# Kernel optimization log

Hardware: AMD Instinct MI355X
Metric: run time of the kernel (lower is better)

## Reference

```python
import jax, jax.numpy as jnp
import numpy as np

SLOPE = 25.0

@jax.custom_vjp
def spike_fn(u):
    return (u > 0).astype(u.dtype)

def _spike_fwd(u):
    return (u > 0).astype(u.dtype), u

def _spike_bwd(u, g):
    # fast-sigmoid surrogate gradient, slope=25 (matches surrogate_slope)
    return (g / (1.0 + SLOPE * jnp.abs(u)) ** 2,)

spike_fn.defvjp(_spike_fwd, _spike_bwd)

B, T, D = 4, 8192, 1024
TREE_DEPTH = 10
NUM_NODES = (1 << TREE_DEPTH) - 1


def setup_inputs() -> dict:
    key = jax.random.key(0)
    k0, k1, k2 = jax.random.split(key, 3)
    x = jax.random.normal(k0, (B, T, D), jnp.float32)
    # torch Linear(2D -> D, bias=False): weight [D, 2D], kaiming-uniform-ish scale
    W_proj = jax.random.normal(k1, (D, 2 * D), jnp.float32) / np.sqrt(2 * D)
    node_weights = jax.random.normal(k2, (NUM_NODES, D), jnp.float32) * 0.02
    bt = jnp.ones((TREE_DEPTH, D), jnp.float32) * 0.5    # base_threshold per level
    as_w = jnp.ones((TREE_DEPTH, D), jnp.float32) * 0.1  # adapt_strength per level
    rms_w = jnp.ones((D,), jnp.float32)                   # RMSNorm weight
    return {"x": x, "W_proj": W_proj, "node_weights": node_weights,
            "bt": bt, "as_w": as_w, "rms_w": rms_w}


def reference(x, W_proj, node_weights, bt, as_w, rms_w):
    b, t, d = x.shape
    tree_depth = bt.shape[0]
    num_nodes = (1 << tree_depth) - 1

    padded_T = 1 << int(np.ceil(np.log2(t)))
    x_p = jnp.pad(x, ((0, 0), (0, padded_T - t), (0, 0))) if padded_T > t else x

    eff_depth = min(tree_depth, int(np.log2(padded_T)))
    num_leaves = 1 << eff_depth
    sub_seq = padded_T // num_leaves
    # [B, num_leaves, D]: mean-pool sub-sequences into leaf states
    leaves = x_p.reshape(b, num_leaves, sub_seq, d).mean(axis=2)

    node_states = jnp.zeros((b, num_nodes, d), x.dtype)
    leaf_start = (1 << (eff_depth - 1)) - 1
    valid = min(num_leaves, num_nodes - leaf_start)
    node_states = node_states.at[:, leaf_start:leaf_start + valid].set(leaves[:, :valid])

    # bottom-up over tree levels (static small loop over eff_depth)
    for level in range(eff_depth - 1, -1, -1):
        level_start = (1 << level) - 1
        level_end = min((1 << (level + 1)) - 1, num_nodes)
        nodes = np.arange(level_start, level_end)
        mask = 2 * nodes + 1 < num_nodes
        if not mask.any():
            continue  # leaf level: children out of range, write is a no-op
        nsel = nodes[mask]
        l_idx = 2 * nsel + 1
        r_idx = 2 * nsel + 2  # always < num_nodes in a full binary tree when l is
        l_states = node_states[:, l_idx]               # [B, n_lvl, D] gather
        r_states = node_states[:, r_idx]
        fused = jnp.concatenate([l_states, r_states], axis=-1)  # [B, n_lvl, 2D]
        proj = jnp.einsum('bne,de->bnd', fused, W_proj)
        # ALIF single step from zero state: v = proj, thresh = bt (adapt = 0)
        u = proj - (bt[level] + as_w[level] * 0.0)
        spike = spike_fn(u)
        node_states = node_states.at[:, nsel].set(proj * spike)

    weights = jax.nn.softmax(node_weights, axis=0)       # softmax over nodes
    mixture = jnp.einsum('nd,bnd->bd', weights, node_states)
    out = mixture[:, None, :] + x_p[:, :t]               # broadcast over T
    # RMSNorm (torch default eps = machine eps for dtype)
    eps = jnp.finfo(x.dtype).eps
    rms = jnp.sqrt(jnp.mean(out * out, axis=-1, keepdims=True) + eps)
    return (out / rms) * rms_w
```

## Files before the change

### kernel.cpp

```cpp
#include <hip/hip_runtime.h>


#define NODES 1023
#define DIM   1024
#define K2    2048
#define NCHUNK 64

typedef short short8 __attribute__((ext_vector_type(8)));
typedef float floatx4 __attribute__((ext_vector_type(4)));

__device__ __forceinline__ unsigned short f2bf(float f) {
    unsigned u = __float_as_uint(f);
    unsigned r = ((u >> 16) & 1u) + 0x7fffu;
    return (unsigned short)((u + r) >> 16);
}

#define GLD16(g, l)                                                            \
    __builtin_amdgcn_global_load_lds(                                          \
        (const __attribute__((address_space(1))) void*)(g),                    \
        (__attribute__((address_space(3))) void*)(l), 16, 0, 0)

__global__ __launch_bounds__(256) void k_cvt_w(const float* __restrict__ W,
                                               unsigned short* __restrict__ Wb) {
    int i = (blockIdx.x * 256 + threadIdx.x) * 4;
    float4 v = *(const float4*)(W + i);
    ushort4 o;
    o.x = f2bf(v.x); o.y = f2bf(v.y); o.z = f2bf(v.z); o.w = f2bf(v.w);
    *(ushort4*)(Wb + i) = o;
}

__global__ __launch_bounds__(256) void k_leaves(const float* __restrict__ x,
                                                float* __restrict__ Sf,
                                                unsigned short* __restrict__ Sb) {
    int leaf = blockIdx.x;
    int b = blockIdx.y;
    int d = threadIdx.x * 4;
    const float* xp = x + ((size_t)b * 8192 + (size_t)leaf * 8) * DIM + d;
    float4 s = {0.f, 0.f, 0.f, 0.f};
#pragma unroll
    for (int i = 0; i < 8; ++i) {
        float4 v = *(const float4*)(xp + (size_t)i * DIM);
        s.x += v.x; s.y += v.y; s.z += v.z; s.w += v.w;
    }
    s.x *= 0.125f; s.y *= 0.125f; s.z *= 0.125f; s.w *= 0.125f;
    size_t o = ((size_t)b * NODES + 511 + leaf) * DIM + d;
    *(float4*)(Sf + o) = s;
    ushort4 ob; ob.x = f2bf(s.x); ob.y = f2bf(s.y); ob.z = f2bf(s.z); ob.w = f2bf(s.w);
    *(ushort4*)(Sb + o) = ob;
}

__global__ __launch_bounds__(256) void k_level_mfma(
    const unsigned short* __restrict__ SbIn, const unsigned short* __restrict__ Wb,
    const float* __restrict__ bt, float* __restrict__ Sf,
    unsigned short* __restrict__ SbOut, float* __restrict__ P,
    int L, int R, int nit) {
    const int lvl_start = (1 << L) - 1;
    const int child_start = (2 << L) - 1;
    const int mask = (1 << L) - 1;

    __shared__ unsigned short Al[2][128 * 64];
    __shared__ unsigned short Bl[2][128 * 64];

    const int t = threadIdx.x;
    const int lane = t & 63;
    const int w = t >> 6;
    const int wm = w >> 1, wn = w & 1;
    const int bm = blockIdx.y, bn = blockIdx.x;
    const int ksid = blockIdx.z;
    const int k_base = ksid * nit * 64;

    floatx4 acc[4][4];
#pragma unroll
    for (int i = 0; i < 4; ++i)
#pragma unroll
        for (int j = 0; j < 4; ++j) acc[i][j] = (floatx4){0.f, 0.f, 0.f, 0.f};

    const int trow = t >> 3;
    const int tcol = (t & 7) * 8;

    const unsigned short* aptr[4];
#pragma unroll
    for (int p = 0; p < 4; ++p) {
        int rg = bm * 128 + p * 32 + trow;
        rg = rg < R ? rg : R - 1;
        int bb = rg >> L;
        int nl = rg & mask;
        aptr[p] = SbIn + ((size_t)bb * NODES + child_start + 2 * nl) * DIM + tcol;
    }
    const unsigned short* bptr[4];
#pragma unroll
    for (int p = 0; p < 4; ++p) {
        int rg = bn * 128 + p * 32 + trow;
        bptr[p] = Wb + (size_t)rg * K2 + tcol;
    }

#define STAGE(buf, k0)                                                         \
    {                                                                          \
        _Pragma("unroll")                                                      \
        for (int p = 0; p < 4; ++p)                                            \
            GLD16(aptr[p] + (k0), &Al[buf][(p * 32 + w * 8) * 64]);            \
        _Pragma("unroll")                                                      \
        for (int p = 0; p < 4; ++p)                                            \
            GLD16(bptr[p] + (k0), &Bl[buf][(p * 32 + w * 8) * 64]);            \
    }

    int cur = 0;
    STAGE(0, k_base);
    asm volatile("s_waitcnt vmcnt(0)" ::: "memory");
    __builtin_amdgcn_s_barrier();

    for (int it = 0; it < nit; ++it) {
        if (it + 1 < nit) STAGE(cur ^ 1, k_base + (it + 1) * 64);
#pragma unroll
        for (int ks = 0; ks < 2; ++ks) {
            short8 af[4], bf[4];
#pragma unroll
            for (int i = 0; i < 4; ++i) {
                af[i] = *(const short8*)&Al[cur][(wm * 64 + i * 16 + (lane & 15)) * 64 +
                                                ks * 32 + (lane >> 4) * 8];
                bf[i] = *(const short8*)&Bl[cur][(wn * 64 + i * 16 + (lane & 15)) * 64 +
                                                ks * 32 + (lane >> 4) * 8];
            }
#pragma unroll
            for (int i = 0; i < 4; ++i)
#pragma unroll
                for (int j = 0; j < 4; ++j)
                    acc[i][j] = __builtin_amdgcn_mfma_f32_16x16x32_bf16(
                        af[i], bf[j], acc[i][j], 0, 0, 0);
        }
        asm volatile("s_waitcnt vmcnt(0)" ::: "memory");
        __builtin_amdgcn_s_barrier();
        cur ^= 1;
    }
#undef STAGE

    if (P) {
        float* Pr = P + (size_t)ksid * R * DIM;
#pragma unroll
        for (int i = 0; i < 4; ++i)
#pragma unroll
            for (int j = 0; j < 4; ++j)
#pragma unroll
                for (int r = 0; r < 4; ++r) {
                    int m = bm * 128 + wm * 64 + i * 16 + (lane >> 4) * 4 + r;
                    int n = bn * 128 + wn * 64 + j * 16 + (lane & 15);
                    if (m < R) Pr[(size_t)m * DIM + n] = acc[i][j][r];
                }
    } else {
#pragma unroll
        for (int i = 0; i < 4; ++i)
#pragma unroll
            for (int j = 0; j < 4; ++j)
#pragma unroll
                for (int r = 0; r < 4; ++r) {
                    int m = bm * 128 + wm * 64 + i * 16 + (lane >> 4) * 4 + r;
                    int n = bn * 128 + wn * 64 + j * 16 + (lane & 15);
                    if (m < R) {
                        float v = acc[i][j][r];
                        float u = v - bt[L * DIM + n];
                        float o = (u > 0.f) ? v : 0.f;
                        int bb = m >> L;
                        int nl = m & mask;
                        size_t idx = ((size_t)bb * NODES + lvl_start + nl) * DIM + n;
                        Sf[idx] = o;
                        SbOut[idx] = f2bf(o);
                    }
                }
    }
}

__global__ __launch_bounds__(256) void k_level_fix(
    const float* __restrict__ P, const float* __restrict__ bt,
    float* __restrict__ Sf, unsigned short* __restrict__ Sb,
    int L, int R, int KS) {
    int m = blockIdx.x;
    int n = threadIdx.x * 4;
    float4 s = {0.f, 0.f, 0.f, 0.f};
    for (int k = 0; k < KS; ++k) {
        float4 v = *(const float4*)(P + ((size_t)k * R + m) * DIM + n);
        s.x += v.x; s.y += v.y; s.z += v.z; s.w += v.w;
    }
    float4 btv = *(const float4*)(bt + (size_t)L * DIM + n);
    float4 o;
    o.x = (s.x - btv.x > 0.f) ? s.x : 0.f;
    o.y = (s.y - btv.y > 0.f) ? s.y : 0.f;
    o.z = (s.z - btv.z > 0.f) ? s.z : 0.f;
    o.w = (s.w - btv.w > 0.f) ? s.w : 0.f;
    int b = m >> L;
    int nl = m & ((1 << L) - 1);
    size_t idx = ((size_t)b * NODES + ((1 << L) - 1) + nl) * DIM + n;
    *(float4*)(Sf + idx) = o;
    ushort4 ob;
    ob.x = f2bf(o.x); ob.y = f2bf(o.y); ob.z = f2bf(o.z); ob.w = f2bf(o.w);
    *(ushort4*)(Sb + idx) = ob;
}

__global__ __launch_bounds__(256) void k_level_small(
    const float* __restrict__ SfIn, const float* __restrict__ W,
    const float* __restrict__ bt, float* __restrict__ Sf,
    unsigned short* __restrict__ Sb, int L) {
    int r = blockIdx.y;
    int b = r >> L;
    int nl = r & ((1 << L) - 1);
    int node = (1 << L) - 1 + nl;
    int child = 2 * node + 1;
    const float* A = SfIn + ((size_t)b * NODES + child) * DIM;

    __shared__ float Alds[K2];
    int t = threadIdx.x;
    ((float4*)Alds)[t * 2] = ((const float4*)A)[t * 2];
    ((float4*)Alds)[t * 2 + 1] = ((const float4*)A)[t * 2 + 1];
    __syncthreads();

    int d = blockIdx.x * 64 + (t & 63);
    int kc = t >> 6;
    const float4* Wr = (const float4*)(W + (size_t)d * K2 + kc * 512);
    const float4* Ar = (const float4*)(Alds + kc * 512);
    float s = 0.f;
#pragma unroll 8
    for (int i = 0; i < 128; ++i) {
        float4 wv = Wr[i], av = Ar[i];
        s += wv.x * av.x + wv.y * av.y + wv.z * av.z + wv.w * av.w;
    }
    __shared__ float part[256];
    part[t] = s;
    __syncthreads();
    if (t < 64) {
        float v = part[t] + part[t + 64] + part[t + 128] + part[t + 192];
        float u = v - bt[L * DIM + d];
        float o = (u > 0.f) ? v : 0.f;
        size_t idx = ((size_t)b * NODES + node) * DIM + d;
        Sf[idx] = o;
        Sb[idx] = f2bf(o);
    }
}

__global__ __launch_bounds__(256) void k_mixture_part(const float* __restrict__ nw,
                                                      const float* __restrict__ Sf,
                                                      float* __restrict__ part) {
    int d = blockIdx.x * 256 + threadIdx.x;
    int c = blockIdx.y;
    int n0i = c * 16;
    int n1i = n0i + 16 < NODES ? n0i + 16 : NODES;
    float denom = 0.f, s0 = 0.f, s1 = 0.f, s2 = 0.f, s3 = 0.f;
    for (int n = n0i; n < n1i; ++n) {
        float wv = __expf(nw[(size_t)n * DIM + d]);
        denom += wv;
        s0 += wv * Sf[((size_t)0 * NODES + n) * DIM + d];
        s1 += wv * Sf[((size_t)1 * NODES + n) * DIM + d];
        s2 += wv * Sf[((size_t)2 * NODES + n) * DIM + d];
        s3 += wv * Sf[((size_t)3 * NODES + n) * DIM + d];
    }
    size_t base = ((size_t)c * 5) * DIM + d;
    part[base]           = denom;
    part[base + 1 * DIM] = s0;
    part[base + 2 * DIM] = s1;
    part[base + 3 * DIM] = s2;
    part[base + 4 * DIM] = s3;
}

__global__ __launch_bounds__(256) void k_mixture_red(const float* __restrict__ part,
                                                     float* __restrict__ mix) {
    int d = blockIdx.x * 256 + threadIdx.x;
    float denom = 0.f, s0 = 0.f, s1 = 0.f, s2 = 0.f, s3 = 0.f;
#pragma unroll 8
    for (int c = 0; c < NCHUNK; ++c) {
        size_t base = ((size_t)c * 5) * DIM + d;
        denom += part[base];
        s0 += part[base + 1 * DIM];
        s1 += part[base + 2 * DIM];
        s2 += part[base + 3 * DIM];
        s3 += part[base + 4 * DIM];
    }
    float inv = 1.f / denom;
    mix[0 * DIM + d] = s0 * inv;
    mix[1 * DIM + d] = s1 * inv;
    mix[2 * DIM + d] = s2 * inv;
    mix[3 * DIM + d] = s3 * inv;
}

__global__ __launch_bounds__(256) void k_final(const float* __restrict__ x,
                                               const float* __restrict__ mix,
                                               const float* __restrict__ rw,
                                               float* __restrict__ out) {
    int row = blockIdx.x;
    int b = row >> 13;
    size_t base = (size_t)row * DIM;
    int t = threadIdx.x;
    float4 xv = *(const float4*)(x + base + t * 4);
    float4 mv = *(const float4*)(mix + b * DIM + t * 4);
    float4 v = {xv.x + mv.x, xv.y + mv.y, xv.z + mv.z, xv.w + mv.w};
    float ss = v.x * v.x + v.y * v.y + v.z * v.z + v.w * v.w;
#pragma unroll
    for (int o = 32; o > 0; o >>= 1) ss += __shfl_xor(ss, o, 64);
    __shared__ float wsum[4];
    int lane = t & 63, wv_ = t >> 6;
    if (lane == 0) wsum[wv_] = ss;
    __syncthreads();
    float tot = wsum[0] + wsum[1] + wsum[2] + wsum[3];
    float inv = 1.f / sqrtf(tot * (1.f / 1024.f) + 1.1920929e-7f);
    float4 rwv = *(const float4*)(rw + t * 4);
    float4 o4 = {v.x * inv * rwv.x, v.y * inv * rwv.y, v.z * inv * rwv.z,
                 v.w * inv * rwv.w};
    *(float4*)(out + base + t * 4) = o4;
}

extern "C" void kernel_launch(void* const* d_in, const int* in_sizes, int n_in,
                              void* d_out, int out_size, void* d_ws, size_t ws_size,
                              hipStream_t stream) {
    (void)in_sizes; (void)n_in; (void)out_size;
    const float* x  = (const float*)d_in[0];
    const float* W  = (const float*)d_in[1];
    const float* nw = (const float*)d_in[2];
    const float* bt = (const float*)d_in[3];
    const float* rw = (const float*)d_in[5];
    float* out = (float*)d_out;

    char* ws = (char*)d_ws;
    const size_t SF_BYTES = (size_t)4 * NODES * DIM * 4;
    const size_t SB_BYTES = (size_t)4 * NODES * DIM * 2;
    const size_t WB_BYTES = (size_t)K2 * DIM * 2;
    const size_t MIX_BYTES = (size_t)4 * DIM * 4;
    const size_t BASE = SF_BYTES + SB_BYTES + WB_BYTES + MIX_BYTES;
    float* Sf = (float*)ws;
    unsigned short* Sb = (unsigned short*)(ws + SF_BYTES);
    unsigned short* Wb = (unsigned short*)(ws + SF_BYTES + SB_BYTES);
    float* mix = (float*)(ws + SF_BYTES + SB_BYTES + WB_BYTES);
    float* P = (float*)(ws + BASE);
    float* part = (float*)(ws + BASE);
    size_t avail = ws_size > BASE ? ws_size - BASE : 0;

    k_cvt_w<<<2048, 256, 0, stream>>>(W, Wb);
    k_leaves<<<dim3(512, 4), 256, 0, stream>>>(x, Sf, Sb);

    for (int L = 8; L >= 4; --L) {
        int R = 4 << L;
        int Mt = (R + 127) / 128;
        int ks = (L == 8) ? 4 : (L == 7) ? 8 : 16;
        while (ks > 1 && (size_t)ks * R * DIM * 4 > avail) ks >>= 1;
        if (ks >= 2 && (size_t)ks * R * DIM * 4 <= avail) {
            int nit = 32 / ks;
            k_level_mfma<<<dim3(8, Mt, ks), 256, 0, stream>>>(
                Sb, Wb, bt, Sf, Sb, P, L, R, nit);
            k_level_fix<<<R, 256, 0, stream>>>(P, bt, Sf, Sb, L, R, ks);
        } else {
            k_level_mfma<<<dim3(8, Mt, 1), 256, 0, stream>>>(
                Sb, Wb, bt, Sf, Sb, nullptr, L, R, 32);
        }
    }
    for (int L = 3; L >= 0; --L) {
        int R = 4 << L;
        k_level_small<<<dim3(16, R), 256, 0, stream>>>(Sf, W, bt, Sf, Sb, L);
    }
    k_mixture_part<<<dim3(4, NCHUNK), 256, 0, stream>>>(nw, Sf, part);
    k_mixture_red<<<4, 256, 0, stream>>>(part, mix);
    k_final<<<32768, 256, 0, stream>>>(x, mix, rw, out);
}
```

Measured before the change: 444.0 us.

## Shrink MFMA tiles to 64x64, add triple-buffered swizzled LDS, fuse prep kernels

Tiles in the per-level bf16 MFMA GEMM shrink from 128x128 to 64x64 with a three-stage LDS ring and partial vmcnt waits, so the next loads overlap compute. An XOR swizzle on LDS columns is meant to cut bank conflicts on fragment reads. Split-K factors are lowered because the smaller tiles already give more blocks. The weight conversion and leaf pooling kernels are merged into one launch. The trade-off is less data reuse per tile, and small levels may still leave the GPU underfilled.

```diff
diff --git a/kernel.cpp b/kernel.cpp
--- a/kernel.cpp
+++ b/kernel.cpp
@@ -20,33 +20,37 @@
         (const __attribute__((address_space(1))) void*)(g),                    \
         (__attribute__((address_space(3))) void*)(l), 16, 0, 0)
 
-__global__ __launch_bounds__(256) void k_cvt_w(const float* __restrict__ W,
-                                               unsigned short* __restrict__ Wb) {
-    int i = (blockIdx.x * 256 + threadIdx.x) * 4;
-    float4 v = *(const float4*)(W + i);
-    ushort4 o;
-    o.x = f2bf(v.x); o.y = f2bf(v.y); o.z = f2bf(v.z); o.w = f2bf(v.w);
-    *(ushort4*)(Wb + i) = o;
-}
-
-__global__ __launch_bounds__(256) void k_leaves(const float* __restrict__ x,
-                                                float* __restrict__ Sf,
-                                                unsigned short* __restrict__ Sb) {
-    int leaf = blockIdx.x;
-    int b = blockIdx.y;
-    int d = threadIdx.x * 4;
-    const float* xp = x + ((size_t)b * 8192 + (size_t)leaf * 8) * DIM + d;
-    float4 s = {0.f, 0.f, 0.f, 0.f};
-#pragma unroll
-    for (int i = 0; i < 8; ++i) {
-        float4 v = *(const float4*)(xp + (size_t)i * DIM);
-        s.x += v.x; s.y += v.y; s.z += v.z; s.w += v.w;
-    }
-    s.x *= 0.125f; s.y *= 0.125f; s.z *= 0.125f; s.w *= 0.125f;
-    size_t o = ((size_t)b * NODES + 511 + leaf) * DIM + d;
-    *(float4*)(Sf + o) = s;
-    ushort4 ob; ob.x = f2bf(s.x); ob.y = f2bf(s.y); ob.z = f2bf(s.z); ob.w = f2bf(s.w);
-    *(ushort4*)(Sb + o) = ob;
+__global__ __launch_bounds__(256) void k_prep(const float* __restrict__ W,
+                                              unsigned short* __restrict__ Wb,
+                                              const float* __restrict__ x,
+                                              float* __restrict__ Sf,
+                                              unsigned short* __restrict__ Sb) {
+    int bx = blockIdx.x;
+    if (bx < 2048) {
+        int i = (bx * 256 + threadIdx.x) * 4;
+        float4 v = *(const float4*)(W + i);
+        ushort4 o;
+        o.x = f2bf(v.x); o.y = f2bf(v.y); o.z = f2bf(v.z); o.w = f2bf(v.w);
+        *(ushort4*)(Wb + i) = o;
+    } else {
+        int idx = bx - 2048;
+        int leaf = idx & 511;
+        int b = idx >> 9;
+        int d = threadIdx.x * 4;
+        const float* xp = x + ((size_t)b * 8192 + (size_t)leaf * 8) * DIM + d;
+        float4 s = {0.f, 0.f, 0.f, 0.f};
+#pragma unroll
+        for (int i = 0; i < 8; ++i) {
+            float4 v = *(const float4*)(xp + (size_t)i * DIM);
+            s.x += v.x; s.y += v.y; s.z += v.z; s.w += v.w;
+        }
+        s.x *= 0.125f; s.y *= 0.125f; s.z *= 0.125f; s.w *= 0.125f;
+        size_t o = ((size_t)b * NODES + 511 + leaf) * DIM + d;
+        *(float4*)(Sf + o) = s;
+        ushort4 ob;
+        ob.x = f2bf(s.x); ob.y = f2bf(s.y); ob.z = f2bf(s.z); ob.w = f2bf(s.w);
+        *(ushort4*)(Sb + o) = ob;
+    }
 }
 
 __global__ __launch_bounds__(256) void k_level_mfma(
@@ -58,8 +62,8 @@
     const int child_start = (2 << L) - 1;
     const int mask = (1 << L) - 1;
 
-    __shared__ unsigned short Al[2][128 * 64];
-    __shared__ unsigned short Bl[2][128 * 64];
+    __shared__ unsigned short Al[3][64 * 64];
+    __shared__ unsigned short Bl[3][64 * 64];
 
     const int t = threadIdx.x;
     const int lane = t & 63;
@@ -69,92 +73,103 @@
     const int ksid = blockIdx.z;
     const int k_base = ksid * nit * 64;
 
-    floatx4 acc[4][4];
-#pragma unroll
-    for (int i = 0; i < 4; ++i)
-#pragma unroll
-        for (int j = 0; j < 4; ++j) acc[i][j] = (floatx4){0.f, 0.f, 0.f, 0.f};
+    floatx4 acc[2][2];
+#pragma unroll
+    for (int i = 0; i < 2; ++i)
+#pragma unroll
+        for (int j = 0; j < 2; ++j) acc[i][j] = (floatx4){0.f, 0.f, 0.f, 0.f};
 
     const int trow = t >> 3;
-    const int tcol = (t & 7) * 8;
-
-    const unsigned short* aptr[4];
-#pragma unroll
-    for (int p = 0; p < 4; ++p) {
-        int rg = bm * 128 + p * 32 + trow;
+    const int csw = ((t & 7) ^ (trow & 7)) * 8;
+
+    const unsigned short* aptr[2];
+#pragma unroll
+    for (int p = 0; p < 2; ++p) {
+        int rg = bm * 64 + p * 32 + trow;
         rg = rg < R ? rg : R - 1;
         int bb = rg >> L;
         int nl = rg & mask;
-        aptr[p] = SbIn + ((size_t)bb * NODES + child_start + 2 * nl) * DIM + tcol;
-    }
-    const unsigned short* bptr[4];
-#pragma unroll
-    for (int p = 0; p < 4; ++p) {
-        int rg = bn * 128 + p * 32 + trow;
-        bptr[p] = Wb + (size_t)rg * K2 + tcol;
+        aptr[p] = SbIn + ((size_t)bb * NODES + child_start + 2 * nl) * DIM + csw;
+    }
+    const unsigned short* bptr[2];
+#pragma unroll
+    for (int p = 0; p < 2; ++p) {
+        int rg = bn * 64 + p * 32 + trow;
+        bptr[p] = Wb + (size_t)rg * K2 + csw;
     }
 
 #define STAGE(buf, k0)                                                         \
     {                                                                          \
         _Pragma("unroll")                                                      \
-        for (int p = 0; p < 4; ++p)                                            \
+        for (int p = 0; p < 2; ++p)                                            \
             GLD16(aptr[p] + (k0), &Al[buf][(p * 32 + w * 8) * 64]);            \
         _Pragma("unroll")                                                      \
-        for (int p = 0; p < 4; ++p)                                            \
+        for (int p = 0; p < 2; ++p)                                            \
             GLD16(bptr[p] + (k0), &Bl[buf][(p * 32 + w * 8) * 64]);            \
     }
 
-    int cur = 0;
+    const int rsel = lane & 15;
+    const int jx = lane >> 4;
+    const int swz = lane & 7;
+
     STAGE(0, k_base);
-    asm volatile("s_waitcnt vmcnt(0)" ::: "memory");
-    __builtin_amdgcn_s_barrier();
+    if (nit > 1) STAGE(1, k_base + 64);
 
     for (int it = 0; it < nit; ++it) {
-        if (it + 1 < nit) STAGE(cur ^ 1, k_base + (it + 1) * 64);
+        if (it + 1 < nit) {
+            asm volatile("s_waitcnt vmcnt(4)" ::: "memory");
+        } else {
+            asm volatile("s_waitcnt vmcnt(0)" ::: "memory");
+        }
+        __builtin_amdgcn_s_barrier();
+        asm volatile("" ::: "memory");
+        if (it + 2 < nit) STAGE((it + 2) % 3, k_base + (it + 2) * 64);
+
+        const char* Ab = (const char*)&Al[it % 3][0];
+        const char* Bb = (const char*)&Bl[it % 3][0];
 #pragma unroll
         for (int ks = 0; ks < 2; ++ks) {
-            short8 af[4], bf[4];
-#pragma unroll
-            for (int i = 0; i < 4; ++i) {
-                af[i] = *(const short8*)&Al[cur][(wm * 64 + i * 16 + (lane & 15)) * 64 +
-                                                ks * 32 + (lane >> 4) * 8];
-                bf[i] = *(const short8*)&Bl[cur][(wn * 64 + i * 16 + (lane & 15)) * 64 +
-                                                ks * 32 + (lane >> 4) * 8];
+            short8 af[2], bf[2];
+#pragma unroll
+            for (int i = 0; i < 2; ++i) {
+                int ar = wm * 32 + i * 16 + rsel;
+                af[i] = *(const short8*)(Ab + ar * 128 +
+                                         (((ks * 4 + jx) ^ swz) << 4));
+                int br = wn * 32 + i * 16 + rsel;
+                bf[i] = *(const short8*)(Bb + br * 128 +
+                                         (((ks * 4 + jx) ^ swz) << 4));
             }
 #pragma unroll
-            for (int i = 0; i < 4; ++i)
-#pragma unroll
-                for (int j = 0; j < 4; ++j)
+            for (int i = 0; i < 2; ++i)
+#pragma unroll
+                for (int j = 0; j < 2; ++j)
                     acc[i][j] = __builtin_amdgcn_mfma_f32_16x16x32_bf16(
                         af[i], bf[j], acc[i][j], 0, 0, 0);
         }
-        asm volatile("s_waitcnt vmcnt(0)" ::: "memory");
-        __builtin_amdgcn_s_barrier();
-        cur ^= 1;
     }
 #undef STAGE
 
     if (P) {
         float* Pr = P + (size_t)ksid * R * DIM;
 #pragma unroll
-        for (int i = 0; i < 4; ++i)
-#pragma unroll
-            for (int j = 0; j < 4; ++j)
+        for (int i = 0; i < 2; ++i)
+#pragma unroll
+            for (int j = 0; j < 2; ++j)
 #pragma unroll
                 for (int r = 0; r < 4; ++r) {
-                    int m = bm * 128 + wm * 64 + i * 16 + (lane >> 4) * 4 + r;
-                    int n = bn * 128 + wn * 64 + j * 16 + (lane & 15);
+                    int m = bm * 64 + wm * 32 + i * 16 + (lane >> 4) * 4 + r;
+                    int n = bn * 64 + wn * 32 + j * 16 + (lane & 15);
                     if (m < R) Pr[(size_t)m * DIM + n] = acc[i][j][r];
                 }
     } else {
 #pragma unroll
-        for (int i = 0; i < 4; ++i)
-#pragma unroll
-            for (int j = 0; j < 4; ++j)
+        for (int i = 0; i < 2; ++i)
+#pragma unroll
+            for (int j = 0; j < 2; ++j)
 #pragma unroll
                 for (int r = 0; r < 4; ++r) {
-                    int m = bm * 128 + wm * 64 + i * 16 + (lane >> 4) * 4 + r;
-                    int n = bn * 128 + wn * 64 + j * 16 + (lane & 15);
+                    int m = bm * 64 + wm * 32 + i * 16 + (lane >> 4) * 4 + r;
+                    int n = bn * 64 + wn * 32 + j * 16 + (lane & 15);
                     if (m < R) {
                         float v = acc[i][j][r];
                         float u = v - bt[L * DIM + n];
@@ -330,21 +345,20 @@
     float* part = (float*)(ws + BASE);
     size_t avail = ws_size > BASE ? ws_size - BASE : 0;
 
-    k_cvt_w<<<2048, 256, 0, stream>>>(W, Wb);
-    k_leaves<<<dim3(512, 4), 256, 0, stream>>>(x, Sf, Sb);
+    k_prep<<<4096, 256, 0, stream>>>(W, Wb, x, Sf, Sb);
 
     for (int L = 8; L >= 4; --L) {
         int R = 4 << L;
-        int Mt = (R + 127) / 128;
-        int ks = (L == 8) ? 4 : (L == 7) ? 8 : 16;
+        int Mt = R / 64;
+        int ks = (L >= 7) ? 2 : (L >= 5) ? 4 : 8;
         while (ks > 1 && (size_t)ks * R * DIM * 4 > avail) ks >>= 1;
-        if (ks >= 2 && (size_t)ks * R * DIM * 4 <= avail) {
-            int nit = 32 / ks;
-            k_level_mfma<<<dim3(8, Mt, ks), 256, 0, stream>>>(
+        int nit = 32 / ks;
+        if (ks >= 2) {
+            k_level_mfma<<<dim3(16, Mt, ks), 256, 0, stream>>>(
                 Sb, Wb, bt, Sf, Sb, P, L, R, nit);
             k_level_fix<<<R, 256, 0, stream>>>(P, bt, Sf, Sb, L, R, ks);
         } else {
-            k_level_mfma<<<dim3(8, Mt, 1), 256, 0, stream>>>(
+            k_level_mfma<<<dim3(16, Mt, 1), 256, 0, stream>>>(
                 Sb, Wb, bt, Sf, Sb, nullptr, L, R, 32);
         }
     }
```

Measured after the change: 420.8 us. 5.2% less time.
